# Kernel optimization log

Measured on AMD Instinct MI355X. Metric: run time of the kernel, lower is better.

## Reference

```python
import jax, jax.numpy as jnp
import numpy as np

N, E, IN, HID, OUT = 40000, 640000, 128, 512, 256


def setup_inputs() -> dict:
    key = jax.random.key(0)
    ks = jax.random.split(key, 8)
    x = jax.random.normal(ks[0], (N, IN), dtype=jnp.float32)
    edge_index = jax.random.randint(ks[1], (2, E), 0, N, dtype=jnp.int64)
    # SAGEConv params: lin_l (applied to aggregated neighbors, with bias),
    # lin_r (applied to root nodes, no bias) -- PyG defaults.
    def lin(k, fin, fout):
        return jax.random.normal(k, (fin, fout), dtype=jnp.float32) / np.sqrt(fin)
    return {
        "x": x,
        "edge_index": edge_index,
        "W1l": lin(ks[2], IN, HID),
        "b1": jnp.zeros((HID,), jnp.float32),
        "W1r": lin(ks[3], IN, HID),
        "W2l": lin(ks[4], HID, OUT),
        "b2": jnp.zeros((OUT,), jnp.float32),
        "W2r": lin(ks[5], HID, OUT),
    }


def _sage_conv(x, src, dst, Wl, b, Wr):
    n = x.shape[0]
    # gather messages from source nodes, mean-aggregate at destination
    msg = x[src]                                            # [E, F]
    agg = jax.ops.segment_sum(msg, dst, num_segments=n)     # [N, F]
    cnt = jax.ops.segment_sum(jnp.ones((src.shape[0],), x.dtype), dst,
                              num_segments=n)               # [N]
    agg = agg / jnp.maximum(cnt, 1.0)[:, None]
    # out = lin_l(mean_neighbors) + lin_r(x)
    return agg @ Wl + b + x @ Wr


def reference(x, edge_index, W1l, b1, W1r, W2l, b2, W2r):
    src, dst = edge_index[0], edge_index[1]
    h = jax.nn.relu(_sage_conv(x, src, dst, W1l, b1, W1r))
    return _sage_conv(h, src, dst, W2l, b2, W2r)
```

## Files before the change

kernel.cpp:

```cpp
#include <hip/hip_runtime.h>


#define N_NODES 40000
#define N_EDGES 640000
#define F_IN 128
#define F_HID 512
#define F_OUT 256
#define NB_SCAN 157

typedef unsigned short ushort_t;
typedef __attribute__((ext_vector_type(8))) short bf16x8;
typedef __attribute__((ext_vector_type(4))) float floatx4;

__device__ __forceinline__ ushort_t f2bf(float f) {
  union { float f; unsigned int u; } x; x.f = f;
  unsigned int r = (x.u + 0x7FFFu + ((x.u >> 16) & 1u)) >> 16;
  return (ushort_t)r;
}
__device__ __forceinline__ float bf2f(ushort_t u) {
  union { unsigned int u; float f; } x; x.u = ((unsigned int)u) << 16;
  return x.f;
}

__global__ void deg_kernel(const int* __restrict__ ei, int* __restrict__ deg) {
  int e = blockIdx.x * blockDim.x + threadIdx.x;
  if (e < N_EDGES) atomicAdd(&deg[ei[N_EDGES + e]], 1);
}

__global__ void scanA_kernel(const int* __restrict__ deg, int* __restrict__ bsum) {
  __shared__ int sdata[256];
  int i = blockIdx.x * 256 + threadIdx.x;
  sdata[threadIdx.x] = (i < N_NODES) ? deg[i] : 0;
  __syncthreads();
  #pragma unroll
  for (int off = 128; off > 0; off >>= 1) {
    if (threadIdx.x < off) sdata[threadIdx.x] += sdata[threadIdx.x + off];
    __syncthreads();
  }
  if (threadIdx.x == 0) bsum[blockIdx.x] = sdata[0];
}

__global__ void scanB_kernel(const int* __restrict__ bsum, int* __restrict__ boff) {
  __shared__ int buf[2][256];
  int tid = threadIdx.x;
  int v = (tid < NB_SCAN) ? bsum[tid] : 0;
  buf[0][tid] = v;
  __syncthreads();
  int cur = 0;
  #pragma unroll
  for (int off = 1; off < 256; off <<= 1) {
    int val = buf[cur][tid];
    if (tid >= off) val += buf[cur][tid - off];
    buf[cur ^ 1][tid] = val;
    __syncthreads();
    cur ^= 1;
  }
  if (tid < NB_SCAN) boff[tid] = buf[cur][tid] - v;
}

__global__ void scanC_kernel(const int* __restrict__ deg, const int* __restrict__ boff,
                             int* __restrict__ rowptr, int* __restrict__ cursor) {
  __shared__ int buf[2][256];
  int tid = threadIdx.x;
  int i = blockIdx.x * 256 + tid;
  int v = (i < N_NODES) ? deg[i] : 0;
  buf[0][tid] = v;
  __syncthreads();
  int cur = 0;
  #pragma unroll
  for (int off = 1; off < 256; off <<= 1) {
    int val = buf[cur][tid];
    if (tid >= off) val += buf[cur][tid - off];
    buf[cur ^ 1][tid] = val;
    __syncthreads();
    cur ^= 1;
  }
  if (i < N_NODES) {
    int ex = boff[blockIdx.x] + buf[cur][tid] - v;
    rowptr[i] = ex;
    cursor[i] = ex;
    if (i == N_NODES - 1) rowptr[N_NODES] = ex + v;
  }
}

__global__ void fill_kernel(const int* __restrict__ ei, int* __restrict__ cursor,
                            int* __restrict__ col) {
  int e = blockIdx.x * blockDim.x + threadIdx.x;
  if (e < N_EDGES) {
    int d = ei[N_EDGES + e];
    int s = ei[e];
    int pos = atomicAdd(&cursor[d], 1);
    col[pos] = s;
  }
}

__global__ void cvt_x_kernel(const float* __restrict__ x, ushort_t* __restrict__ xb) {
  int i = blockIdx.x * blockDim.x + threadIdx.x;
  const int n4 = (N_NODES * F_IN) / 4;
  if (i < n4) {
    float4 v = ((const float4*)x)[i];
    ushort4 o;
    o.x = f2bf(v.x); o.y = f2bf(v.y); o.z = f2bf(v.z); o.w = f2bf(v.w);
    ((ushort4*)xb)[i] = o;
  }
}

__global__ void wt_kernel(const float* __restrict__ W, ushort_t* __restrict__ Wt,
                          int K, int N, int rowoff, int koff, int ldt) {
  int i = blockIdx.x * blockDim.x + threadIdx.x;
  if (i < K * N) {
    int n = i / K, k = i - n * K;
    Wt[(size_t)(rowoff + n) * ldt + koff + k] = f2bf(W[(size_t)k * N + n]);
  }
}

__global__ void biascat_kernel(const float* __restrict__ b2, float* __restrict__ bc) {
  int i = threadIdx.x + blockIdx.x * blockDim.x;
  if (i < 512) bc[i] = (i < 256) ? 0.f : b2[i - 256];
}

__global__ void agg1_kernel(const ushort_t* __restrict__ Xb, ushort_t* __restrict__ Yb,
                            const int* __restrict__ rowptr, const int* __restrict__ colidx) {
  __shared__ int cols[64];
  int n = blockIdx.x, f = threadIdx.x;
  int s = rowptr[n], e = rowptr[n + 1];
  float s0 = 0.f, s1 = 0.f;
  for (int base = s; base < e; base += 64) {
    int cnt = min(64, e - base);
    __syncthreads();
    if (f < cnt) cols[f] = colidx[base + f];
    __syncthreads();
    for (int j = 0; j < cnt; ++j) {
      unsigned int v = *(const unsigned int*)(Xb + (size_t)cols[j] * F_IN + 2 * f);
      s0 += bf2f((ushort_t)(v & 0xffffu));
      s1 += bf2f((ushort_t)(v >> 16));
    }
  }
  float inv = 1.f / fmaxf((float)(e - s), 1.f);
  unsigned int o = (unsigned int)f2bf(s0 * inv) | ((unsigned int)f2bf(s1 * inv) << 16);
  *(unsigned int*)(Yb + (size_t)n * F_IN + 2 * f) = o;
}

__global__ void agg2_kernel(const ushort_t* __restrict__ hl, const float* __restrict__ hr,
                            float* __restrict__ out,
                            const int* __restrict__ rowptr, const int* __restrict__ colidx) {
  __shared__ int cols[128];
  int n = blockIdx.x, f = threadIdx.x;
  int s = rowptr[n], e = rowptr[n + 1];
  float s0 = 0.f, s1 = 0.f;
  for (int base = s; base < e; base += 128) {
    int cnt = min(128, e - base);
    __syncthreads();
    if (f < cnt) cols[f] = colidx[base + f];
    __syncthreads();
    for (int j = 0; j < cnt; ++j) {
      unsigned int v = *(const unsigned int*)(hl + (size_t)cols[j] * F_OUT + 2 * f);
      s0 += bf2f((ushort_t)(v & 0xffffu));
      s1 += bf2f((ushort_t)(v >> 16));
    }
  }
  float inv = 1.f / fmaxf((float)(e - s), 1.f);
  float2 hrv = *(const float2*)(hr + (size_t)n * F_OUT + 2 * f);
  float2 o;
  o.x = s0 * inv + hrv.x;
  o.y = s1 * inv + hrv.y;
  *(float2*)(out + (size_t)n * F_OUT + 2 * f) = o;
}

template <bool TWOPAIR, bool RELU, bool BIAS, bool OUT_BF16, bool SPLITOUT, int KT>
__global__ __launch_bounds__(256) void gemm_mfma(
    const ushort_t* __restrict__ A0, const ushort_t* __restrict__ A1,
    const ushort_t* __restrict__ Wt, const float* __restrict__ bias,
    float* __restrict__ Cf, ushort_t* __restrict__ Cb, int M) {
  const int BM = 64, BN = 256;
  const int NKC = KT / 8;
  __shared__ ushort_t Apan[64 * KT];
  const int tid = threadIdx.x;
  const int wave = tid >> 6, lane = tid & 63;
  const int lm = lane & 15, qk = lane >> 4;
  const int bn = blockIdx.x * BN;
  const int bm = blockIdx.y * BM;
  const int K0 = TWOPAIR ? KT / 2 : KT;
  const int K0c = K0 / 8;

  #pragma unroll
  for (int q = 0; q < (64 * NKC) / 256; ++q) {
    int c = tid + q * 256;
    int kc = c & (NKC - 1);
    int row = c / NKC;
    const ushort_t* src = (TWOPAIR && kc >= K0c)
        ? A1 + (size_t)(bm + row) * K0 + (kc - K0c) * 8
        : A0 + (size_t)(bm + row) * K0 + kc * 8;
    bf16x8 v = *(const bf16x8*)src;
    size_t off = ((size_t)(kc * 64 + row) * 16) ^ (size_t)((kc & 7) << 4);
    *(bf16x8*)((char*)Apan + off) = v;
  }

  const ushort_t* bp = Wt + (size_t)(bn + wave * 64 + lm) * KT + qk * 8;
  bf16x8 bvA[4], bvB[4];
  #pragma unroll
  for (int ni = 0; ni < 4; ++ni)
    bvA[ni] = *(const bf16x8*)(bp + (size_t)ni * 16 * KT);

  __syncthreads();

  floatx4 acc[4][4] = {};
  #pragma unroll 1
  for (int kb = 0; kb < KT; kb += 64) {
    #pragma unroll
    for (int ni = 0; ni < 4; ++ni)
      bvB[ni] = *(const bf16x8*)(bp + (size_t)ni * 16 * KT + kb + 32);

    bf16x8 av[4];
    const int kc0 = kb / 8 + qk;
    #pragma unroll
    for (int mi = 0; mi < 4; ++mi) {
      size_t off = ((size_t)(kc0 * 64 + mi * 16 + lm) * 16) ^ (size_t)((kc0 & 7) << 4);
      av[mi] = *(const bf16x8*)((char*)Apan + off);
    }
    #pragma unroll
    for (int mi = 0; mi < 4; ++mi)
      #pragma unroll
      for (int ni = 0; ni < 4; ++ni)
        acc[mi][ni] = __builtin_amdgcn_mfma_f32_16x16x32_bf16(
            bvA[ni], av[mi], acc[mi][ni], 0, 0, 0);

    if (kb + 64 < KT) {
      #pragma unroll
      for (int ni = 0; ni < 4; ++ni)
        bvA[ni] = *(const bf16x8*)(bp + (size_t)ni * 16 * KT + kb + 64);
    }

    const int kc1 = kb / 8 + 4 + qk;
    #pragma unroll
    for (int mi = 0; mi < 4; ++mi) {
      size_t off = ((size_t)(kc1 * 64 + mi * 16 + lm) * 16) ^ (size_t)((kc1 & 7) << 4);
      av[mi] = *(const bf16x8*)((char*)Apan + off);
    }
    #pragma unroll
    for (int mi = 0; mi < 4; ++mi)
      #pragma unroll
      for (int ni = 0; ni < 4; ++ni)
        acc[mi][ni] = __builtin_amdgcn_mfma_f32_16x16x32_bf16(
            bvB[ni], av[mi], acc[mi][ni], 0, 0, 0);
  }

  #pragma unroll
  for (int ni = 0; ni < 4; ++ni) {
    int colg = bn + wave * 64 + ni * 16 + qk * 4;
    float4 b4 = {0.f, 0.f, 0.f, 0.f};
    if (BIAS) b4 = *(const float4*)&bias[colg];
    #pragma unroll
    for (int mi = 0; mi < 4; ++mi) {
      int rowg = bm + mi * 16 + lm;
      float v0 = acc[mi][ni][0] + b4.x;
      float v1 = acc[mi][ni][1] + b4.y;
      float v2 = acc[mi][ni][2] + b4.z;
      float v3 = acc[mi][ni][3] + b4.w;
      if (RELU) {
        v0 = fmaxf(v0, 0.f); v1 = fmaxf(v1, 0.f);
        v2 = fmaxf(v2, 0.f); v3 = fmaxf(v3, 0.f);
      }
      if (SPLITOUT) {
        if (colg < 256) {
          ushort4 o = {f2bf(v0), f2bf(v1), f2bf(v2), f2bf(v3)};
          *(ushort4*)&Cb[(size_t)rowg * 256 + colg] = o;
        } else {
          float4 o = {v0, v1, v2, v3};
          *(float4*)&Cf[(size_t)rowg * 256 + (colg - 256)] = o;
        }
      } else if (OUT_BF16) {
        ushort4 o = {f2bf(v0), f2bf(v1), f2bf(v2), f2bf(v3)};
        *(ushort4*)&Cb[(size_t)rowg * 512 + colg] = o;
      } else {
        float4 o = {v0, v1, v2, v3};
        *(float4*)&Cf[(size_t)rowg * 512 + colg] = o;
      }
    }
  }
}

extern "C" void kernel_launch(void* const* d_in, const int* in_sizes, int n_in,
                              void* d_out, int out_size, void* d_ws, size_t ws_size,
                              hipStream_t stream) {
  const float* x = (const float*)d_in[0];
  const int* ei = (const int*)d_in[1];
  const float* W1l = (const float*)d_in[2];
  const float* b1 = (const float*)d_in[3];
  const float* W1r = (const float*)d_in[4];
  const float* W2l = (const float*)d_in[5];
  const float* b2 = (const float*)d_in[6];
  const float* W2r = (const float*)d_in[7];
  float* out = (float*)d_out;

  char* ws = (char*)d_ws;
  size_t off = 0;
  auto alloc = [&](size_t bytes) {
    void* p = ws + off;
    off = (off + bytes + 255) & ~(size_t)255;
    return p;
  };
  int* deg = (int*)alloc((size_t)N_NODES * 4);
  int* rowptr = (int*)alloc((size_t)(N_NODES + 1) * 4);
  int* cursor = (int*)alloc((size_t)N_NODES * 4);
  int* col = (int*)alloc((size_t)N_EDGES * 4);
  int* bsum = (int*)alloc((size_t)NB_SCAN * 4);
  int* boff = (int*)alloc((size_t)NB_SCAN * 4);
  ushort_t* x_bf = (ushort_t*)alloc((size_t)N_NODES * F_IN * 2);
  ushort_t* aggx_bf = (ushort_t*)alloc((size_t)N_NODES * F_IN * 2);
  ushort_t* h_bf = (ushort_t*)alloc((size_t)N_NODES * F_HID * 2);
  ushort_t* hl_bf = (ushort_t*)alloc((size_t)N_NODES * F_OUT * 2);
  float* hr = (float*)alloc((size_t)N_NODES * F_OUT * 4);
  ushort_t* Wcat1t = (ushort_t*)alloc((size_t)512 * 256 * 2);
  ushort_t* Wcatt = (ushort_t*)alloc((size_t)512 * F_HID * 2);
  float* biascat = (float*)alloc(512 * 4);

  hipMemsetAsync(deg, 0, (size_t)N_NODES * 4, stream);
  deg_kernel<<<(N_EDGES + 255) / 256, 256, 0, stream>>>(ei, deg);
  scanA_kernel<<<NB_SCAN, 256, 0, stream>>>(deg, bsum);
  scanB_kernel<<<1, 256, 0, stream>>>(bsum, boff);
  scanC_kernel<<<NB_SCAN, 256, 0, stream>>>(deg, boff, rowptr, cursor);
  fill_kernel<<<(N_EDGES + 255) / 256, 256, 0, stream>>>(ei, cursor, col);

  cvt_x_kernel<<<(N_NODES * F_IN / 4 + 255) / 256, 256, 0, stream>>>(x, x_bf);
  wt_kernel<<<(F_IN * F_HID + 255) / 256, 256, 0, stream>>>(W1l, Wcat1t, 128, 512, 0, 0, 256);
  wt_kernel<<<(F_IN * F_HID + 255) / 256, 256, 0, stream>>>(W1r, Wcat1t, 128, 512, 0, 128, 256);
  wt_kernel<<<(F_HID * F_OUT + 255) / 256, 256, 0, stream>>>(W2l, Wcatt, 512, 256, 0, 0, 512);
  wt_kernel<<<(F_HID * F_OUT + 255) / 256, 256, 0, stream>>>(W2r, Wcatt, 512, 256, 256, 0, 512);
  biascat_kernel<<<2, 256, 0, stream>>>(b2, biascat);

  agg1_kernel<<<N_NODES, 64, 0, stream>>>(x_bf, aggx_bf, rowptr, col);
  gemm_mfma<true, true, true, true, false, 256>
      <<<dim3(2, N_NODES / 64), 256, 0, stream>>>(
          aggx_bf, x_bf, Wcat1t, b1, nullptr, h_bf, N_NODES);

  gemm_mfma<false, false, true, false, true, 512>
      <<<dim3(2, N_NODES / 64), 256, 0, stream>>>(
          h_bf, nullptr, Wcatt, biascat, hr, hl_bf, N_NODES);
  agg2_kernel<<<N_NODES, 128, 0, stream>>>(hl_bf, hr, out, rowptr, col);
}
```

Measured before the change: 339.4 us.

## Pre-pack weights into MFMA fragment layout, split A panel, unroll gathers

Weights are now written by a packing kernel into the per-lane MFMA fragment order, so each wave reads B with contiguous 512-byte loads instead of row-strided ones. For K=512 the GEMM stages the A panel in two 256-wide halves, halving LDS use (to 32 KB) so more blocks fit per CU, at the cost of extra barriers. Both aggregation kernels unroll the neighbour gather by four to keep more independent loads in flight.

```diff
diff --git a/kernel.cpp b/kernel.cpp
--- a/kernel.cpp
+++ b/kernel.cpp
@@ -105,12 +105,16 @@
   }
 }
 
-__global__ void wt_kernel(const float* __restrict__ W, ushort_t* __restrict__ Wt,
-                          int K, int N, int rowoff, int koff, int ldt) {
+__global__ void wp_kernel(const float* __restrict__ W, ushort_t* __restrict__ Wp,
+                          int K, int N, int rowoff, int koff, int KT) {
   int i = blockIdx.x * blockDim.x + threadIdx.x;
   if (i < K * N) {
     int n = i / K, k = i - n * K;
-    Wt[(size_t)(rowoff + n) * ldt + koff + k] = f2bf(W[(size_t)k * N + n]);
+    int ng = rowoff + n, kg = koff + k;
+    int gg = ng >> 6, ni = (ng >> 4) & 3, lm = ng & 15;
+    int c = kg >> 3, j = kg & 7, t = c >> 2, qk = c & 3;
+    size_t dst = (((size_t)(gg * (KT / 32) + t) * 4 + ni) * 64 + qk * 16 + lm) * 8 + j;
+    Wp[dst] = f2bf(W[(size_t)k * N + n]);
   }
 }
 
@@ -130,7 +134,18 @@
     __syncthreads();
     if (f < cnt) cols[f] = colidx[base + f];
     __syncthreads();
-    for (int j = 0; j < cnt; ++j) {
+    int j = 0;
+    for (; j + 4 <= cnt; j += 4) {
+      unsigned int v0 = *(const unsigned int*)(Xb + (size_t)cols[j + 0] * F_IN + 2 * f);
+      unsigned int v1 = *(const unsigned int*)(Xb + (size_t)cols[j + 1] * F_IN + 2 * f);
+      unsigned int v2 = *(const unsigned int*)(Xb + (size_t)cols[j + 2] * F_IN + 2 * f);
+      unsigned int v3 = *(const unsigned int*)(Xb + (size_t)cols[j + 3] * F_IN + 2 * f);
+      s0 += bf2f((ushort_t)(v0 & 0xffffu)) + bf2f((ushort_t)(v1 & 0xffffu)) +
+            bf2f((ushort_t)(v2 & 0xffffu)) + bf2f((ushort_t)(v3 & 0xffffu));
+      s1 += bf2f((ushort_t)(v0 >> 16)) + bf2f((ushort_t)(v1 >> 16)) +
+            bf2f((ushort_t)(v2 >> 16)) + bf2f((ushort_t)(v3 >> 16));
+    }
+    for (; j < cnt; ++j) {
       unsigned int v = *(const unsigned int*)(Xb + (size_t)cols[j] * F_IN + 2 * f);
       s0 += bf2f((ushort_t)(v & 0xffffu));
       s1 += bf2f((ushort_t)(v >> 16));
@@ -153,7 +168,18 @@
     __syncthreads();
     if (f < cnt) cols[f] = colidx[base + f];
     __syncthreads();
-    for (int j = 0; j < cnt; ++j) {
+    int j = 0;
+    for (; j + 4 <= cnt; j += 4) {
+      unsigned int v0 = *(const unsigned int*)(hl + (size_t)cols[j + 0] * F_OUT + 2 * f);
+      unsigned int v1 = *(const unsigned int*)(hl + (size_t)cols[j + 1] * F_OUT + 2 * f);
+      unsigned int v2 = *(const unsigned int*)(hl + (size_t)cols[j + 2] * F_OUT + 2 * f);
+      unsigned int v3 = *(const unsigned int*)(hl + (size_t)cols[j + 3] * F_OUT + 2 * f);
+      s0 += bf2f((ushort_t)(v0 & 0xffffu)) + bf2f((ushort_t)(v1 & 0xffffu)) +
+            bf2f((ushort_t)(v2 & 0xffffu)) + bf2f((ushort_t)(v3 & 0xffffu));
+      s1 += bf2f((ushort_t)(v0 >> 16)) + bf2f((ushort_t)(v1 >> 16)) +
+            bf2f((ushort_t)(v2 >> 16)) + bf2f((ushort_t)(v3 >> 16));
+    }
+    for (; j < cnt; ++j) {
       unsigned int v = *(const unsigned int*)(hl + (size_t)cols[j] * F_OUT + 2 * f);
       s0 += bf2f((ushort_t)(v & 0xffffu));
       s1 += bf2f((ushort_t)(v >> 16));
@@ -170,79 +196,93 @@
 template <bool TWOPAIR, bool RELU, bool BIAS, bool OUT_BF16, bool SPLITOUT, int KT>
 __global__ __launch_bounds__(256) void gemm_mfma(
     const ushort_t* __restrict__ A0, const ushort_t* __restrict__ A1,
-    const ushort_t* __restrict__ Wt, const float* __restrict__ bias,
+    const ushort_t* __restrict__ Wp, const float* __restrict__ bias,
     float* __restrict__ Cf, ushort_t* __restrict__ Cb, int M) {
-  const int BM = 64, BN = 256;
-  const int NKC = KT / 8;
-  __shared__ ushort_t Apan[64 * KT];
+  const int KH = (KT > 256) ? 256 : KT;
+  const int NH = KT / KH;
+  const int NKH = KH / 8;
+  __shared__ ushort_t Apan[64 * KH];
   const int tid = threadIdx.x;
   const int wave = tid >> 6, lane = tid & 63;
   const int lm = lane & 15, qk = lane >> 4;
-  const int bn = blockIdx.x * BN;
-  const int bm = blockIdx.y * BM;
+  const int bn = blockIdx.x * 256;
+  const int bm = blockIdx.y * 64;
   const int K0 = TWOPAIR ? KT / 2 : KT;
   const int K0c = K0 / 8;
 
-  #pragma unroll
-  for (int q = 0; q < (64 * NKC) / 256; ++q) {
-    int c = tid + q * 256;
-    int kc = c & (NKC - 1);
-    int row = c / NKC;
-    const ushort_t* src = (TWOPAIR && kc >= K0c)
-        ? A1 + (size_t)(bm + row) * K0 + (kc - K0c) * 8
-        : A0 + (size_t)(bm + row) * K0 + kc * 8;
-    bf16x8 v = *(const bf16x8*)src;
-    size_t off = ((size_t)(kc * 64 + row) * 16) ^ (size_t)((kc & 7) << 4);
-    *(bf16x8*)((char*)Apan + off) = v;
-  }
-
-  const ushort_t* bp = Wt + (size_t)(bn + wave * 64 + lm) * KT + qk * 8;
+  const ushort_t* wpg = Wp + (size_t)(blockIdx.x * 4 + wave) * (KT / 32) * 2048;
+
+  auto stageA = [&](int h) {
+    #pragma unroll
+    for (int q = 0; q < (64 * NKH) / 256; ++q) {
+      int c = tid + q * 256;
+      int lc = c & (NKH - 1);
+      int row = c / NKH;
+      int kc = h * NKH + lc;
+      const ushort_t* src = (TWOPAIR && kc >= K0c)
+          ? A1 + (size_t)(bm + row) * K0 + (kc - K0c) * 8
+          : A0 + (size_t)(bm + row) * K0 + kc * 8;
+      bf16x8 v = *(const bf16x8*)src;
+      size_t off = ((size_t)(lc * 64 + row) * 16) ^ (size_t)((lc & 7) << 4);
+      *(bf16x8*)((char*)Apan + off) = v;
+    }
+  };
+
+  stageA(0);
   bf16x8 bvA[4], bvB[4];
   #pragma unroll
   for (int ni = 0; ni < 4; ++ni)
-    bvA[ni] = *(const bf16x8*)(bp + (size_t)ni * 16 * KT);
-
+    bvA[ni] = *(const bf16x8*)(wpg + (size_t)ni * 512 + lane * 8);
   __syncthreads();
 
   floatx4 acc[4][4] = {};
   #pragma unroll 1
-  for (int kb = 0; kb < KT; kb += 64) {
-    #pragma unroll
-    for (int ni = 0; ni < 4; ++ni)
-      bvB[ni] = *(const bf16x8*)(bp + (size_t)ni * 16 * KT + kb + 32);
-
-    bf16x8 av[4];
-    const int kc0 = kb / 8 + qk;
-    #pragma unroll
-    for (int mi = 0; mi < 4; ++mi) {
-      size_t off = ((size_t)(kc0 * 64 + mi * 16 + lm) * 16) ^ (size_t)((kc0 & 7) << 4);
-      av[mi] = *(const bf16x8*)((char*)Apan + off);
-    }
-    #pragma unroll
-    for (int mi = 0; mi < 4; ++mi)
+  for (int h = 0; h < NH; ++h) {
+    if (h) {
+      __syncthreads();
+      stageA(h);
+      __syncthreads();
+    }
+    #pragma unroll 1
+    for (int kb = 0; kb < KH; kb += 64) {
+      const int t0 = (h * KH + kb) / 32;
       #pragma unroll
       for (int ni = 0; ni < 4; ++ni)
-        acc[mi][ni] = __builtin_amdgcn_mfma_f32_16x16x32_bf16(
-            bvA[ni], av[mi], acc[mi][ni], 0, 0, 0);
-
-    if (kb + 64 < KT) {
-      #pragma unroll
-      for (int ni = 0; ni < 4; ++ni)
-        bvA[ni] = *(const bf16x8*)(bp + (size_t)ni * 16 * KT + kb + 64);
-    }
-
-    const int kc1 = kb / 8 + 4 + qk;
-    #pragma unroll
-    for (int mi = 0; mi < 4; ++mi) {
-      size_t off = ((size_t)(kc1 * 64 + mi * 16 + lm) * 16) ^ (size_t)((kc1 & 7) << 4);
-      av[mi] = *(const bf16x8*)((char*)Apan + off);
-    }
-    #pragma unroll
-    for (int mi = 0; mi < 4; ++mi)
-      #pragma unroll
-      for (int ni = 0; ni < 4; ++ni)
-        acc[mi][ni] = __builtin_amdgcn_mfma_f32_16x16x32_bf16(
-            bvB[ni], av[mi], acc[mi][ni], 0, 0, 0);
+        bvB[ni] = *(const bf16x8*)(wpg + ((size_t)(t0 + 1) * 4 + ni) * 512 + lane * 8);
+
+      bf16x8 av[4];
+      const int kc0 = kb / 8 + qk;
+      #pragma unroll
+      for (int mi = 0; mi < 4; ++mi) {
+        size_t off = ((size_t)(kc0 * 64 + mi * 16 + lm) * 16) ^ (size_t)((kc0 & 7) << 4);
+        av[mi] = *(const bf16x8*)((char*)Apan + off);
+      }
+      #pragma unroll
+      for (int mi = 0; mi < 4; ++mi)
+        #pragma unroll
+        for (int ni = 0; ni < 4; ++ni)
+          acc[mi][ni] = __builtin_amdgcn_mfma_f32_16x16x32_bf16(
+              bvA[ni], av[mi], acc[mi][ni], 0, 0, 0);
+
+      if (h * KH + kb + 64 < KT) {
+        #pragma unroll
+        for (int ni = 0; ni < 4; ++ni)
+          bvA[ni] = *(const bf16x8*)(wpg + ((size_t)(t0 + 2) * 4 + ni) * 512 + lane * 8);
+      }
+
+      const int kc1 = kb / 8 + 4 + qk;
+      #pragma unroll
+      for (int mi = 0; mi < 4; ++mi) {
+        size_t off = ((size_t)(kc1 * 64 + mi * 16 + lm) * 16) ^ (size_t)((kc1 & 7) << 4);
+        av[mi] = *(const bf16x8*)((char*)Apan + off);
+      }
+      #pragma unroll
+      for (int mi = 0; mi < 4; ++mi)
+        #pragma unroll
+        for (int ni = 0; ni < 4; ++ni)
+          acc[mi][ni] = __builtin_amdgcn_mfma_f32_16x16x32_bf16(
+              bvB[ni], av[mi], acc[mi][ni], 0, 0, 0);
+    }
   }
 
   #pragma unroll
@@ -311,8 +351,8 @@
   ushort_t* h_bf = (ushort_t*)alloc((size_t)N_NODES * F_HID * 2);
   ushort_t* hl_bf = (ushort_t*)alloc((size_t)N_NODES * F_OUT * 2);
   float* hr = (float*)alloc((size_t)N_NODES * F_OUT * 4);
-  ushort_t* Wcat1t = (ushort_t*)alloc((size_t)512 * 256 * 2);
-  ushort_t* Wcatt = (ushort_t*)alloc((size_t)512 * F_HID * 2);
+  ushort_t* Wp1 = (ushort_t*)alloc((size_t)512 * 256 * 2);
+  ushort_t* Wp2 = (ushort_t*)alloc((size_t)512 * 512 * 2);
   float* biascat = (float*)alloc(512 * 4);
 
   hipMemsetAsync(deg, 0, (size_t)N_NODES * 4, stream);
@@ -323,19 +363,19 @@
   fill_kernel<<<(N_EDGES + 255) / 256, 256, 0, stream>>>(ei, cursor, col);
 
   cvt_x_kernel<<<(N_NODES * F_IN / 4 + 255) / 256, 256, 0, stream>>>(x, x_bf);
-  wt_kernel<<<(F_IN * F_HID + 255) / 256, 256, 0, stream>>>(W1l, Wcat1t, 128, 512, 0, 0, 256);
-  wt_kernel<<<(F_IN * F_HID + 255) / 256, 256, 0, stream>>>(W1r, Wcat1t, 128, 512, 0, 128, 256);
-  wt_kernel<<<(F_HID * F_OUT + 255) / 256, 256, 0, stream>>>(W2l, Wcatt, 512, 256, 0, 0, 512);
-  wt_kernel<<<(F_HID * F_OUT + 255) / 256, 256, 0, stream>>>(W2r, Wcatt, 512, 256, 256, 0, 512);
+  wp_kernel<<<(F_IN * F_HID + 255) / 256, 256, 0, stream>>>(W1l, Wp1, 128, 512, 0, 0, 256);
+  wp_kernel<<<(F_IN * F_HID + 255) / 256, 256, 0, stream>>>(W1r, Wp1, 128, 512, 0, 128, 256);
+  wp_kernel<<<(F_HID * F_OUT + 255) / 256, 256, 0, stream>>>(W2l, Wp2, 512, 256, 0, 0, 512);
+  wp_kernel<<<(F_HID * F_OUT + 255) / 256, 256, 0, stream>>>(W2r, Wp2, 512, 256, 256, 0, 512);
   biascat_kernel<<<2, 256, 0, stream>>>(b2, biascat);
 
   agg1_kernel<<<N_NODES, 64, 0, stream>>>(x_bf, aggx_bf, rowptr, col);
   gemm_mfma<true, true, true, true, false, 256>
       <<<dim3(2, N_NODES / 64), 256, 0, stream>>>(
-          aggx_bf, x_bf, Wcat1t, b1, nullptr, h_bf, N_NODES);
+          aggx_bf, x_bf, Wp1, b1, nullptr, h_bf, N_NODES);
 
   gemm_mfma<false, false, true, false, true, 512>
       <<<dim3(2, N_NODES / 64), 256, 0, stream>>>(
-          h_bf, nullptr, Wcatt, biascat, hr, hl_bf, N_NODES);
+          h_bf, nullptr, Wp2, biascat, hr, hl_bf, N_NODES);
   agg2_kernel<<<N_NODES, 128, 0, stream>>>(hl_bf, hr, out, rowptr, col);
 }
```

New measurement: 307.6 us. -9.4%, faster.
